# Kernel optimization log

Measured on AMD Instinct MI355X. Metric: run time of the kernel, lower is better.

Reference implementation:

```python
import jax, jax.numpy as jnp
import numpy as np

E, H, HD = 2048, 32, 64
SCALE = HD ** -0.5


def setup_inputs() -> dict:
    key = jax.random.key(0)
    ks = jax.random.split(key, 11)
    B, T, P = 16, 4, 4096
    S = P + T
    return {
        "hidden_states": jax.random.normal(ks[0], (B, T, E), jnp.float32),
        "past_key": jax.random.normal(ks[1], (1, H, P, HD), jnp.float32),
        "past_value": jax.random.normal(ks[2], (1, H, P, HD), jnp.float32),
        "attention_mask": jnp.zeros((B, 1, T, S), jnp.float32),
        "Wq": jax.random.normal(ks[3], (E, E), jnp.float32) * 0.02,
        "bq": jax.random.normal(ks[4], (E,), jnp.float32) * 0.02,
        "Wk": jax.random.normal(ks[5], (E, E), jnp.float32) * 0.02,
        "bk": jax.random.normal(ks[6], (E,), jnp.float32) * 0.02,
        "Wv": jax.random.normal(ks[7], (E, E), jnp.float32) * 0.02,
        "bv": jax.random.normal(ks[8], (E,), jnp.float32) * 0.02,
        "Wo": jax.random.normal(ks[9], (E, E), jnp.float32) * 0.02,
        "bo": jax.random.normal(ks[10], (E,), jnp.float32) * 0.02,
    }


def _shape(x, B, S):
    # [B,S,E] -> [B,H,S,hd]
    return x.reshape(B, S, H, HD).transpose(0, 2, 1, 3)


def reference(hidden_states, past_key, past_value, attention_mask,
              Wq, bq, Wk, bk, Wv, bv, Wo, bo):
    B, T, _ = hidden_states.shape
    # projections (torch Linear: x @ W.T + b); query pre-scaled
    q = _shape(hidden_states @ Wq.T + bq, B, T) * SCALE   # [B,H,T,hd]
    k_new = _shape(hidden_states @ Wk.T + bk, B, T)       # [B,H,T,hd]
    v_new = _shape(hidden_states @ Wv.T + bv, B, T)
    # cache stored with batch 1, broadcast (torch repeat) to B, then concat
    k_past = jnp.broadcast_to(past_key, (B,) + past_key.shape[1:])
    v_past = jnp.broadcast_to(past_value, (B,) + past_value.shape[1:])
    k = jnp.concatenate([k_past, k_new], axis=2)          # [B,H,S,hd]
    v = jnp.concatenate([v_past, v_new], axis=2)
    scores = jnp.einsum('bhtd,bhsd->bhts', q, k)          # [B,H,T,S]
    scores = scores + attention_mask                      # mask is [B,1,T,S]
    scores = jnp.maximum(scores, jnp.finfo(scores.dtype).min)
    w = jax.nn.softmax(scores, axis=-1)
    out = jnp.einsum('bhts,bhsd->bhtd', w, v)             # [B,H,T,hd]
    out = out.transpose(0, 2, 1, 3).reshape(B, T, E)
    return out @ Wo.T + bo
```

## Files before the change

### kernel.cpp

```cpp
#include <hip/hip_runtime.h>


typedef float f4 __attribute__((ext_vector_type(4)));
typedef short s8v __attribute__((ext_vector_type(8)));

#define NEG_HUGE (-3.402823466e38f)

__device__ inline unsigned short f2bs(float x) {
  union { float f; unsigned int u; } a; a.f = x;
  unsigned int u = a.u;
  u += 0x7fffu + ((u >> 16) & 1u);
  return (unsigned short)(u >> 16);
}
__device__ inline float bs2f(unsigned short s) {
  union { unsigned int u; float f; } a; a.u = ((unsigned int)s) << 16;
  return a.f;
}
__device__ inline unsigned long long pack4(float a, float b, float c, float d) {
  return (unsigned long long)f2bs(a) | ((unsigned long long)f2bs(b) << 16)
       | ((unsigned long long)f2bs(c) << 32) | ((unsigned long long)f2bs(d) << 48);
}
__device__ inline s8v cvt8(f4 a, f4 b) {
  s8v r;
  r[0]=(short)f2bs(a[0]); r[1]=(short)f2bs(a[1]); r[2]=(short)f2bs(a[2]); r[3]=(short)f2bs(a[3]);
  r[4]=(short)f2bs(b[0]); r[5]=(short)f2bs(b[1]); r[6]=(short)f2bs(b[2]); r[7]=(short)f2bs(b[3]);
  return r;
}
__device__ inline f4 mfma16(s8v a, s8v b, f4 c) {
  return __builtin_amdgcn_mfma_f32_16x16x32_bf16(a, b, c, 0, 0, 0);
}
__device__ inline f4 fzero() { f4 z = {0.f,0.f,0.f,0.f}; return z; }
__device__ inline float wave_sum(float v) {
  #pragma unroll
  for (int off = 32; off; off >>= 1) v += __shfl_xor(v, off, 64);
  return v;
}

__global__ __launch_bounds__(256) void k_qkv(
    const float* __restrict__ hs, const float* __restrict__ Wq,
    const float* __restrict__ Wk, const float* __restrict__ Wv,
    float* __restrict__ part) {
  __shared__ __align__(16) unsigned short As[64 * 264];
  const int n0 = blockIdx.x * 64;
  const int ksb = blockIdx.y;
  const int p = n0 >> 11;
  const int c0 = n0 & 2047;
  const float* W = (p == 0) ? Wq : (p == 1) ? Wk : Wv;
  const int t = threadIdx.x, lane = t & 63, w = t >> 6;
  const int cl = lane & 15, quad = lane >> 4;

  f4 acc[4];
  #pragma unroll
  for (int i = 0; i < 4; ++i) acc[i] = fzero();

  const int cw = c0 + w * 16 + cl;
  for (int kt = 0; kt < 2; ++kt) {
    const int k0 = ksb * 512 + kt * 256;
    __syncthreads();
    #pragma unroll
    for (int i = 0; i < 16; ++i) {
      int idx4 = t + (i << 8);
      int row = idx4 >> 6;
      int col = (idx4 & 63) << 2;
      f4 v = *reinterpret_cast<const f4*>(hs + row * 2048 + k0 + col);
      *reinterpret_cast<unsigned long long*>(&As[row * 264 + col]) =
          pack4(v[0], v[1], v[2], v[3]);
    }
    __syncthreads();
    const float* wbase = W + (size_t)cw * 2048 + k0;
    #pragma unroll
    for (int ks2 = 0; ks2 < 8; ++ks2) {
      const int kb = ks2 * 32 + quad * 8;
      f4 w0 = *reinterpret_cast<const f4*>(wbase + kb);
      f4 w1 = *reinterpret_cast<const f4*>(wbase + kb + 4);
      s8v bf = cvt8(w0, w1);
      #pragma unroll
      for (int mt = 0; mt < 4; ++mt) {
        s8v af = *reinterpret_cast<const s8v*>(&As[(mt * 16 + cl) * 264 + kb]);
        acc[mt] = mfma16(af, bf, acc[mt]);
      }
    }
  }
  float* outp = part + (size_t)ksb * 64 * 6144;
  #pragma unroll
  for (int mt = 0; mt < 4; ++mt)
    #pragma unroll
    for (int rg = 0; rg < 4; ++rg) {
      int r = mt * 16 + quad * 4 + rg;
      outp[r * 6144 + n0 + w * 16 + cl] = acc[mt][rg];
    }
}

__global__ __launch_bounds__(256) void k_qkv_red(
    const float* __restrict__ part, const float* __restrict__ bq,
    const float* __restrict__ bk, const float* __restrict__ bv,
    unsigned short* __restrict__ qws, float* __restrict__ knew,
    float* __restrict__ vnew) {
  int idx = blockIdx.x * 256 + threadIdx.x;
  int r = idx / 6144;
  int n = idx - r * 6144;
  float s = part[idx] + part[idx + 393216] + part[idx + 786432] + part[idx + 1179648];
  int c = n & 2047, p = n >> 11;
  int h = c >> 6, d = c & 63;
  int b = r >> 2, tt = r & 3;
  if (p == 0) {
    s = (s + bq[c]) * 0.125f;
    qws[h * 4608 + r * 72 + d] = f2bs(s);
  } else if (p == 1) {
    knew[((h * 16 + b) * 4 + tt) * 64 + d] = s + bk[c];
  } else {
    vnew[((h * 16 + b) * 4 + tt) * 64 + d] = s + bv[c];
  }
}

__global__ __launch_bounds__(256) void k_flash(
    const unsigned short* __restrict__ qws, const float* __restrict__ Kp,
    const float* __restrict__ Vp, const float* __restrict__ mask,
    float* __restrict__ Opart, float* __restrict__ mpart,
    float* __restrict__ lpart) {
  __shared__ __align__(16) unsigned short Qs[64 * 72];
  __shared__ __align__(16) float SC[64 * 260];
  __shared__ float mrow[64];
  __shared__ float red[256];
  const int bx = blockIdx.x;
  const int h = bx & 31, cch = bx >> 5;
  const int s0 = cch * 256;
  const int t = threadIdx.x, lane = t & 63, w = t >> 6;
  const int cl = lane & 15, quad = lane >> 4;
  const float* Kh = Kp + (size_t)h * 4096 * 64;
  const float* Vh = Vp + (size_t)h * 4096 * 64;

  {
    const uint4* s4 = reinterpret_cast<const uint4*>(qws + h * 4608);
    uint4* d4 = reinterpret_cast<uint4*>(Qs);
    for (int i = t; i < 576; i += 256) d4[i] = s4[i];
  }
  __syncthreads();

  s8v afr[4][2];
  #pragma unroll
  for (int mt = 0; mt < 4; ++mt)
    #pragma unroll
    for (int k2 = 0; k2 < 2; ++k2)
      afr[mt][k2] = *reinterpret_cast<const s8v*>(
          &Qs[(mt * 16 + cl) * 72 + k2 * 32 + quad * 8]);

  #pragma unroll
  for (int ni = 0; ni < 4; ++ni) {
    const int nt = w * 4 + ni;
    const int srow = s0 + nt * 16 + cl;
    const float* kr = Kh + (size_t)srow * 64 + quad * 8;
    f4 qa[4];
    #pragma unroll
    for (int mt = 0; mt < 4; ++mt) qa[mt] = fzero();
    #pragma unroll
    for (int k2 = 0; k2 < 2; ++k2) {
      f4 k0v = *reinterpret_cast<const f4*>(kr + k2 * 32);
      f4 k1v = *reinterpret_cast<const f4*>(kr + k2 * 32 + 4);
      s8v bf = cvt8(k0v, k1v);
      #pragma unroll
      for (int mt = 0; mt < 4; ++mt) qa[mt] = mfma16(afr[mt][k2], bf, qa[mt]);
    }
    #pragma unroll
    for (int mt = 0; mt < 4; ++mt)
      #pragma unroll
      for (int rg = 0; rg < 4; ++rg) {
        int r = mt * 16 + quad * 4 + rg;
        int sl = nt * 16 + cl;
        float v = qa[mt][rg] + mask[(size_t)r * 4100 + s0 + sl];
        SC[r * 260 + sl] = fmaxf(v, NEG_HUGE);
      }
  }
  __syncthreads();

  {
    const int r = lane, base = w * 64;
    float mx = NEG_HUGE;
    #pragma unroll
    for (int j = 0; j < 64; j += 4) {
      f4 v = *reinterpret_cast<const f4*>(&SC[r * 260 + base + j]);
      mx = fmaxf(fmaxf(fmaxf(mx, v[0]), v[1]), fmaxf(v[2], v[3]));
    }
    red[w * 64 + r] = mx;
  }
  __syncthreads();
  if (t < 64) {
    float m = fmaxf(fmaxf(red[t], red[64 + t]), fmaxf(red[128 + t], red[192 + t]));
    mrow[t] = m;
    mpart[(h * 16 + cch) * 64 + t] = m;
  }
  __syncthreads();
  {
    const int r = lane, base = w * 64;
    const float m = mrow[r];
    float sum = 0.f;
    #pragma unroll
    for (int j = 0; j < 64; j += 4) {
      f4 v = *reinterpret_cast<f4*>(&SC[r * 260 + base + j]);
      f4 e;
      e[0] = __expf(v[0] - m); e[1] = __expf(v[1] - m);
      e[2] = __expf(v[2] - m); e[3] = __expf(v[3] - m);
      *reinterpret_cast<f4*>(&SC[r * 260 + base + j]) = e;
      sum += e[0] + e[1] + e[2] + e[3];
    }
    red[w * 64 + r] = sum;
  }
  __syncthreads();
  if (t < 64)
    lpart[(h * 16 + cch) * 64 + t] = red[t] + red[64 + t] + red[128 + t] + red[192 + t];
  __syncthreads();

  f4 oacc[4];
  #pragma unroll
  for (int mt = 0; mt < 4; ++mt) oacc[mt] = fzero();
  const int dcol = w * 16 + cl;
  #pragma unroll
  for (int k2 = 0; k2 < 8; ++k2) {
    const int sb = k2 * 32 + quad * 8;
    s8v bf;
    #pragma unroll
    for (int j = 0; j < 8; ++j)
      bf[j] = (short)f2bs(Vh[(size_t)(s0 + sb + j) * 64 + dcol]);
    #pragma unroll
    for (int mt = 0; mt < 4; ++mt) {
      const int row = mt * 16 + cl;
      f4 p0 = *reinterpret_cast<const f4*>(&SC[row * 260 + sb]);
      f4 p1 = *reinterpret_cast<const f4*>(&SC[row * 260 + sb + 4]);
      oacc[mt] = mfma16(cvt8(p0, p1), bf, oacc[mt]);
    }
  }
  float* ob = Opart + (size_t)(h * 16 + cch) * 64 * 64;
  #pragma unroll
  for (int mt = 0; mt < 4; ++mt)
    #pragma unroll
    for (int rg = 0; rg < 4; ++rg) {
      int r = mt * 16 + quad * 4 + rg;
      ob[r * 64 + dcol] = oacc[mt][rg];
    }
}

__global__ __launch_bounds__(64) void k_merge(
    const unsigned short* __restrict__ qws, const float* __restrict__ knew,
    const float* __restrict__ vnew, const float* __restrict__ mask,
    const float* __restrict__ Opart, const float* __restrict__ mpart,
    const float* __restrict__ lpart, unsigned short* __restrict__ attn) {
  const int bx = blockIdx.x;
  const int h = bx & 31, b = bx >> 5;
  const int d = threadIdx.x;
  for (int tt = 0; tt < 4; ++tt) {
    const int r = b * 4 + tt;
    float qd = bs2f(qws[h * 4608 + r * 72 + d]);
    float scn[4];
    #pragma unroll
    for (int tp = 0; tp < 4; ++tp) {
      float kn = knew[((h * 16 + b) * 4 + tp) * 64 + d];
      float s = wave_sum(qd * kn);
      s += mask[(size_t)r * 4100 + 4096 + tp];
      scn[tp] = fmaxf(s, NEG_HUGE);
    }
    float mi[16], li[16];
    float mtot = NEG_HUGE;
    #pragma unroll
    for (int i = 0; i < 16; ++i) {
      mi[i] = mpart[(h * 16 + i) * 64 + r];
      li[i] = lpart[(h * 16 + i) * 64 + r];
      mtot = fmaxf(mtot, mi[i]);
    }
    #pragma unroll
    for (int tp = 0; tp < 4; ++tp) mtot = fmaxf(mtot, scn[tp]);
    float ltot = 0.f, od = 0.f;
    #pragma unroll
    for (int i = 0; i < 16; ++i) {
      float fct = __expf(mi[i] - mtot);
      ltot += li[i] * fct;
      od += Opart[((size_t)(h * 16 + i) * 64 + r) * 64 + d] * fct;
    }
    #pragma unroll
    for (int tp = 0; tp < 4; ++tp) {
      float e = __expf(scn[tp] - mtot);
      ltot += e;
      od += e * vnew[((h * 16 + b) * 4 + tp) * 64 + d];
    }
    attn[(size_t)r * 2048 + h * 64 + d] = f2bs(od / ltot);
  }
}

__global__ __launch_bounds__(256) void k_out(
    const unsigned short* __restrict__ attn, const float* __restrict__ Wo,
    float* __restrict__ part) {
  __shared__ __align__(16) unsigned short As[64 * 264];
  const int n0 = blockIdx.x * 64;
  const int ksb = blockIdx.y;
  const int k0 = ksb * 256;
  const int t = threadIdx.x, lane = t & 63, w = t >> 6;
  const int cl = lane & 15, quad = lane >> 4;
  #pragma unroll
  for (int i = 0; i < 8; ++i) {
    int idx8 = t + (i << 8);
    int row = idx8 >> 5;
    int col = (idx8 & 31) << 3;
    *reinterpret_cast<uint4*>(&As[row * 264 + col]) =
        *reinterpret_cast<const uint4*>(attn + (size_t)row * 2048 + k0 + col);
  }
  __syncthreads();
  f4 acc[4];
  #pragma unroll
  for (int i = 0; i < 4; ++i) acc[i] = fzero();
  const int cw = n0 + w * 16 + cl;
  const float* wbase = Wo + (size_t)cw * 2048 + k0;
  #pragma unroll
  for (int ks2 = 0; ks2 < 8; ++ks2) {
    const int kb = ks2 * 32 + quad * 8;
    f4 w0 = *reinterpret_cast<const f4*>(wbase + kb);
    f4 w1 = *reinterpret_cast<const f4*>(wbase + kb + 4);
    s8v bf = cvt8(w0, w1);
    #pragma unroll
    for (int mt = 0; mt < 4; ++mt) {
      s8v af = *reinterpret_cast<const s8v*>(&As[(mt * 16 + cl) * 264 + kb]);
      acc[mt] = mfma16(af, bf, acc[mt]);
    }
  }
  float* op = part + (size_t)ksb * 64 * 2048;
  #pragma unroll
  for (int mt = 0; mt < 4; ++mt)
    #pragma unroll
    for (int rg = 0; rg < 4; ++rg) {
      int r = mt * 16 + quad * 4 + rg;
      op[r * 2048 + n0 + w * 16 + cl] = acc[mt][rg];
    }
}

__global__ __launch_bounds__(256) void k_out_red(
    const float* __restrict__ part, const float* __restrict__ bo,
    float* __restrict__ out) {
  int idx = blockIdx.x * 256 + threadIdx.x;
  int n = idx & 2047;
  float s = bo[n];
  #pragma unroll
  for (int ks = 0; ks < 8; ++ks) s += part[idx + ks * 131072];
  out[idx] = s;
}

extern "C" void kernel_launch(void* const* d_in, const int* in_sizes, int n_in,
                              void* d_out, int out_size, void* d_ws, size_t ws_size,
                              hipStream_t stream) {
  const float* hs   = (const float*)d_in[0];
  const float* pk   = (const float*)d_in[1];
  const float* pv   = (const float*)d_in[2];
  const float* mask = (const float*)d_in[3];
  const float* Wq   = (const float*)d_in[4];
  const float* bq   = (const float*)d_in[5];
  const float* Wk   = (const float*)d_in[6];
  const float* bk   = (const float*)d_in[7];
  const float* Wv   = (const float*)d_in[8];
  const float* bv   = (const float*)d_in[9];
  const float* Wo   = (const float*)d_in[10];
  const float* bo   = (const float*)d_in[11];

  float* f = (float*)d_ws;
  float* qkv_part = f;
  float* o_part   = qkv_part + 1572864;
  float* Opart    = o_part   + 1048576;
  float* mpart    = Opart    + 2097152;
  float* lpart    = mpart    + 32768;
  float* knew     = lpart    + 32768;
  float* vnew     = knew     + 131072;
  unsigned short* qws  = (unsigned short*)(vnew + 131072);
  unsigned short* attn = qws + 147456;

  k_qkv<<<dim3(96, 4), 256, 0, stream>>>(hs, Wq, Wk, Wv, qkv_part);
  k_qkv_red<<<1536, 256, 0, stream>>>(qkv_part, bq, bk, bv, qws, knew, vnew);
  k_flash<<<512, 256, 0, stream>>>(qws, pk, pv, mask, Opart, mpart, lpart);
  k_merge<<<512, 64, 0, stream>>>(qws, knew, vnew, mask, Opart, mpart, lpart, attn);
  k_out<<<dim3(32, 8), 256, 0, stream>>>(attn, Wo, o_part);
  k_out_red<<<512, 256, 0, stream>>>(o_part, bo, (float*)d_out);
}
```

Measured before the change: 213.2 us.

## Keep attention scores in registers and store bf16 probabilities in LDS

The flash kernel now computes S^T tiles (K as the A operand), applies mask and max in registers with wave shuffles, and writes only bf16 exp values to a smaller LDS buffer. This removes the fp32 score round trip through LDS and the separate max/exp passes along with their barriers. The Q fragment is loaded directly from global memory instead of being staged in LDS. The float-to-bf16 conversion now uses the packed HIP intrinsic, and the mask is read as vectors.

```diff
diff --git a/kernel.cpp b/kernel.cpp
--- a/kernel.cpp
+++ b/kernel.cpp
@@ -1,4 +1,5 @@
 #include <hip/hip_runtime.h>
+#include <hip/hip_bf16.h>
 
 
 typedef float f4 __attribute__((ext_vector_type(4)));
@@ -16,15 +17,19 @@
   union { unsigned int u; float f; } a; a.u = ((unsigned int)s) << 16;
   return a.f;
 }
+__device__ inline unsigned int pk2(float a, float b) {
+  union { __hip_bfloat162 v; unsigned int u; } c;
+  c.v = __float22bfloat162_rn(make_float2(a, b));
+  return c.u;
+}
 __device__ inline unsigned long long pack4(float a, float b, float c, float d) {
-  return (unsigned long long)f2bs(a) | ((unsigned long long)f2bs(b) << 16)
-       | ((unsigned long long)f2bs(c) << 32) | ((unsigned long long)f2bs(d) << 48);
+  return (unsigned long long)pk2(a, b) | ((unsigned long long)pk2(c, d) << 32);
 }
 __device__ inline s8v cvt8(f4 a, f4 b) {
-  s8v r;
-  r[0]=(short)f2bs(a[0]); r[1]=(short)f2bs(a[1]); r[2]=(short)f2bs(a[2]); r[3]=(short)f2bs(a[3]);
-  r[4]=(short)f2bs(b[0]); r[5]=(short)f2bs(b[1]); r[6]=(short)f2bs(b[2]); r[7]=(short)f2bs(b[3]);
-  return r;
+  union { s8v s; unsigned int u[4]; } r;
+  r.u[0] = pk2(a[0], a[1]); r.u[1] = pk2(a[2], a[3]);
+  r.u[2] = pk2(b[0], b[1]); r.u[3] = pk2(b[2], b[3]);
+  return r.s;
 }
 __device__ inline f4 mfma16(s8v a, s8v b, f4 c) {
   return __builtin_amdgcn_mfma_f32_16x16x32_bf16(a, b, c, 0, 0, 0);
@@ -118,10 +123,9 @@
     const float* __restrict__ Vp, const float* __restrict__ mask,
     float* __restrict__ Opart, float* __restrict__ mpart,
     float* __restrict__ lpart) {
-  __shared__ __align__(16) unsigned short Qs[64 * 72];
-  __shared__ __align__(16) float SC[64 * 260];
-  __shared__ float mrow[64];
-  __shared__ float red[256];
+  __shared__ __align__(16) unsigned short Pl[64 * 264];
+  __shared__ float redm[4 * 64];
+  __shared__ float reds[4 * 64];
   const int bx = blockIdx.x;
   const int h = bx & 31, cch = bx >> 5;
   const int s0 = cch * 256;
@@ -130,85 +134,97 @@
   const float* Kh = Kp + (size_t)h * 4096 * 64;
   const float* Vh = Vp + (size_t)h * 4096 * 64;
 
-  {
-    const uint4* s4 = reinterpret_cast<const uint4*>(qws + h * 4608);
-    uint4* d4 = reinterpret_cast<uint4*>(Qs);
-    for (int i = t; i < 576; i += 256) d4[i] = s4[i];
-  }
-  __syncthreads();
-
-  s8v afr[4][2];
-  #pragma unroll
-  for (int mt = 0; mt < 4; ++mt)
+  s8v qf[4][2];
+  #pragma unroll
+  for (int qt = 0; qt < 4; ++qt)
     #pragma unroll
     for (int k2 = 0; k2 < 2; ++k2)
-      afr[mt][k2] = *reinterpret_cast<const s8v*>(
-          &Qs[(mt * 16 + cl) * 72 + k2 * 32 + quad * 8]);
-
-  #pragma unroll
-  for (int ni = 0; ni < 4; ++ni) {
-    const int nt = w * 4 + ni;
-    const int srow = s0 + nt * 16 + cl;
-    const float* kr = Kh + (size_t)srow * 64 + quad * 8;
-    f4 qa[4];
-    #pragma unroll
-    for (int mt = 0; mt < 4; ++mt) qa[mt] = fzero();
+      qf[qt][k2] = *reinterpret_cast<const s8v*>(
+          qws + h * 4608 + (qt * 16 + cl) * 72 + k2 * 32 + quad * 8);
+
+  f4 acc[4][4];
+  #pragma unroll
+  for (int si = 0; si < 4; ++si)
+    #pragma unroll
+    for (int qt = 0; qt < 4; ++qt) acc[si][qt] = fzero();
+
+  #pragma unroll
+  for (int si = 0; si < 4; ++si) {
+    const float* kr = Kh + (size_t)(s0 + w * 64 + si * 16 + cl) * 64 + quad * 8;
     #pragma unroll
     for (int k2 = 0; k2 < 2; ++k2) {
       f4 k0v = *reinterpret_cast<const f4*>(kr + k2 * 32);
       f4 k1v = *reinterpret_cast<const f4*>(kr + k2 * 32 + 4);
-      s8v bf = cvt8(k0v, k1v);
-      #pragma unroll
-      for (int mt = 0; mt < 4; ++mt) qa[mt] = mfma16(afr[mt][k2], bf, qa[mt]);
-    }
-    #pragma unroll
-    for (int mt = 0; mt < 4; ++mt)
+      s8v ak = cvt8(k0v, k1v);
+      #pragma unroll
+      for (int qt = 0; qt < 4; ++qt)
+        acc[si][qt] = mfma16(ak, qf[qt][k2], acc[si][qt]);
+    }
+  }
+
+  #pragma unroll
+  for (int si = 0; si < 4; ++si)
+    #pragma unroll
+    for (int qt = 0; qt < 4; ++qt) {
+      f4 mv = *reinterpret_cast<const f4*>(
+          mask + (size_t)(qt * 16 + cl) * 4100 + s0 + w * 64 + si * 16 + quad * 4);
+      #pragma unroll
+      for (int rg = 0; rg < 4; ++rg)
+        acc[si][qt][rg] = fmaxf(acc[si][qt][rg] + mv[rg], NEG_HUGE);
+    }
+
+  #pragma unroll
+  for (int qt = 0; qt < 4; ++qt) {
+    float m = NEG_HUGE;
+    #pragma unroll
+    for (int si = 0; si < 4; ++si)
+      #pragma unroll
+      for (int rg = 0; rg < 4; ++rg) m = fmaxf(m, acc[si][qt][rg]);
+    m = fmaxf(m, __shfl_xor(m, 16, 64));
+    m = fmaxf(m, __shfl_xor(m, 32, 64));
+    if (quad == 0) redm[w * 64 + qt * 16 + cl] = m;
+  }
+  __syncthreads();
+
+  float mq[4];
+  #pragma unroll
+  for (int qt = 0; qt < 4; ++qt) {
+    int q = qt * 16 + cl;
+    mq[qt] = fmaxf(fmaxf(redm[q], redm[64 + q]),
+                   fmaxf(redm[128 + q], redm[192 + q]));
+    if (w == 0 && quad == 0) mpart[(h * 16 + cch) * 64 + q] = mq[qt];
+  }
+  #pragma unroll
+  for (int qt = 0; qt < 4; ++qt) {
+    float sum = 0.f;
+    #pragma unroll
+    for (int si = 0; si < 4; ++si) {
+      f4 e;
       #pragma unroll
       for (int rg = 0; rg < 4; ++rg) {
-        int r = mt * 16 + quad * 4 + rg;
-        int sl = nt * 16 + cl;
-        float v = qa[mt][rg] + mask[(size_t)r * 4100 + s0 + sl];
-        SC[r * 260 + sl] = fmaxf(v, NEG_HUGE);
+        e[rg] = __expf(acc[si][qt][rg] - mq[qt]);
+        sum += e[rg];
       }
+      uint2 pw;
+      pw.x = pk2(e[0], e[1]);
+      pw.y = pk2(e[2], e[3]);
+      *reinterpret_cast<uint2*>(
+          &Pl[(qt * 16 + cl) * 264 + w * 64 + si * 16 + quad * 4]) = pw;
+    }
+    sum += __shfl_xor(sum, 16, 64);
+    sum += __shfl_xor(sum, 32, 64);
+    if (quad == 0) reds[w * 64 + qt * 16 + cl] = sum;
   }
   __syncthreads();
 
-  {
-    const int r = lane, base = w * 64;
-    float mx = NEG_HUGE;
-    #pragma unroll
-    for (int j = 0; j < 64; j += 4) {
-      f4 v = *reinterpret_cast<const f4*>(&SC[r * 260 + base + j]);
-      mx = fmaxf(fmaxf(fmaxf(mx, v[0]), v[1]), fmaxf(v[2], v[3]));
-    }
-    red[w * 64 + r] = mx;
-  }
-  __syncthreads();
-  if (t < 64) {
-    float m = fmaxf(fmaxf(red[t], red[64 + t]), fmaxf(red[128 + t], red[192 + t]));
-    mrow[t] = m;
-    mpart[(h * 16 + cch) * 64 + t] = m;
-  }
-  __syncthreads();
-  {
-    const int r = lane, base = w * 64;
-    const float m = mrow[r];
-    float sum = 0.f;
-    #pragma unroll
-    for (int j = 0; j < 64; j += 4) {
-      f4 v = *reinterpret_cast<f4*>(&SC[r * 260 + base + j]);
-      f4 e;
-      e[0] = __expf(v[0] - m); e[1] = __expf(v[1] - m);
-      e[2] = __expf(v[2] - m); e[3] = __expf(v[3] - m);
-      *reinterpret_cast<f4*>(&SC[r * 260 + base + j]) = e;
-      sum += e[0] + e[1] + e[2] + e[3];
-    }
-    red[w * 64 + r] = sum;
-  }
-  __syncthreads();
-  if (t < 64)
-    lpart[(h * 16 + cch) * 64 + t] = red[t] + red[64 + t] + red[128 + t] + red[192 + t];
-  __syncthreads();
+  if (w == 0 && quad == 0) {
+    #pragma unroll
+    for (int qt = 0; qt < 4; ++qt) {
+      int q = qt * 16 + cl;
+      lpart[(h * 16 + cch) * 64 + q] =
+          reds[q] + reds[64 + q] + reds[128 + q] + reds[192 + q];
+    }
+  }
 
   f4 oacc[4];
   #pragma unroll
@@ -217,26 +233,23 @@
   #pragma unroll
   for (int k2 = 0; k2 < 8; ++k2) {
     const int sb = k2 * 32 + quad * 8;
-    s8v bf;
-    #pragma unroll
-    for (int j = 0; j < 8; ++j)
-      bf[j] = (short)f2bs(Vh[(size_t)(s0 + sb + j) * 64 + dcol]);
+    const float* vb = Vh + (size_t)(s0 + sb) * 64 + dcol;
+    f4 v0, v1;
+    v0[0] = vb[0];   v0[1] = vb[64];  v0[2] = vb[128]; v0[3] = vb[192];
+    v1[0] = vb[256]; v1[1] = vb[320]; v1[2] = vb[384]; v1[3] = vb[448];
+    s8v bv = cvt8(v0, v1);
     #pragma unroll
     for (int mt = 0; mt < 4; ++mt) {
-      const int row = mt * 16 + cl;
-      f4 p0 = *reinterpret_cast<const f4*>(&SC[row * 260 + sb]);
-      f4 p1 = *reinterpret_cast<const f4*>(&SC[row * 260 + sb + 4]);
-      oacc[mt] = mfma16(cvt8(p0, p1), bf, oacc[mt]);
+      s8v pa = *reinterpret_cast<const s8v*>(&Pl[(mt * 16 + cl) * 264 + sb]);
+      oacc[mt] = mfma16(pa, bv, oacc[mt]);
     }
   }
   float* ob = Opart + (size_t)(h * 16 + cch) * 64 * 64;
   #pragma unroll
   for (int mt = 0; mt < 4; ++mt)
     #pragma unroll
-    for (int rg = 0; rg < 4; ++rg) {
-      int r = mt * 16 + quad * 4 + rg;
-      ob[r * 64 + dcol] = oacc[mt][rg];
-    }
+    for (int rg = 0; rg < 4; ++rg)
+      ob[(mt * 16 + quad * 4 + rg) * 64 + dcol] = oacc[mt][rg];
 }
 
 __global__ __launch_bounds__(64) void k_merge(
```

Measured after the change: 210.3 us. Within noise of the previous version (-1.4%).
